# Performance work log

Hardware: AMD Instinct MI355X
Metric: run time of the kernel (lower is better)

The kernel has to match this reference:

```python
import jax, jax.numpy as jnp
import numpy as np

B, S, D = 4, 4096, 1024   # batch, seq_len, d_model
E, K, H = 8, 2, 2048      # num_experts, top_k, expert hidden dim


def setup_inputs() -> dict:
    key = jax.random.key(0)
    k0, k1, k2, k3, k4 = jax.random.split(key, 5)
    scale = 0.02
    return {
        "x": jax.random.normal(k0, (B, S, D), jnp.float32),
        "gate_w": jax.random.normal(k1, (D, E), jnp.float32) * scale,      # nn.Linear(d_model, E, bias=False)
        "w_gate": jax.random.normal(k2, (E, D, H), jnp.float32) * scale,   # expert SwiGLU gate proj
        "w_up":   jax.random.normal(k3, (E, D, H), jnp.float32) * scale,   # expert up proj
        "w_down": jax.random.normal(k4, (E, H, D), jnp.float32) * scale,   # expert down proj
    }


def reference(x, gate_w, w_gate, w_up, w_down):
    b, s, d = x.shape
    e = gate_w.shape[1]
    x_flat = x.reshape(-1, d)                          # [T, D], T = B*S

    gate_logits = x_flat @ gate_w                      # [T, E] (eval mode: no noise)
    top_logits, top_idx = jax.lax.top_k(gate_logits, K)  # [T, K]
    top_w = jax.nn.softmax(top_logits.astype(jnp.float32), axis=1).astype(x.dtype)  # [T, K]

    # load-balancing aux loss (Switch/Mixtral style)
    f_i = jax.nn.one_hot(top_idx, e, dtype=jnp.float32).sum(axis=1).mean(axis=0)  # [E]
    p_i = jax.nn.softmax(gate_logits, axis=1).mean(axis=0)                        # [E]
    aux_loss = (f_i * p_i).sum() * (e ** 2)

    flat_idx = top_idx.reshape(-1)                     # [T*K] expert ids
    # pre-scale token copies by routing weight (matches original)
    y = (x_flat[:, None, :] * top_w[:, :, None]).reshape(-1, d)  # [T*K, D]

    expert_out = jnp.zeros_like(y)
    for i in range(e):  # fixed small expert count: dense-fallback masked MLP
        h = jax.nn.silu(y @ w_gate[i]) * (y @ w_up[i])           # [T*K, H]
        o_i = h @ w_down[i]                                      # [T*K, D]
        expert_out = jnp.where((flat_idx == i)[:, None], o_i, expert_out)

    # faithful to original: scatter_add indexed by EXPERT id (as written in source)
    final = jnp.zeros_like(x_flat).at[flat_idx].add(expert_out)  # [T, D]
    return final.reshape(b, s, d), aux_loss
```

## Files before the change

### kernel.cpp

```cpp
#include <hip/hip_runtime.h>
#include <hip/hip_bf16.h>
#include <stdint.h>

#define T_TOK  16384
#define DMODEL 1024
#define NEXP   8
#define HDIM   2048
#define CAPSL  16512

#define BM 128
#define BN 128
#define NWORK_MAX 264
#define YROWS_MAX (NWORK_MAX*BM)
#define GRID_GEMM (NWORK_MAX * 16)

#define OFF_COUNTS 0
#define OFF_NWORK  64
#define OFF_FSUM   128
#define OFF_PSUM   192
#define OFF_WORK   256
#define OFF_HSUM   8192
#define OFF_ZERO_END 73728
#define OFF_TOK    131072
#define OFF_WGT    786432
#define OFF_WT     2097152
#define WT_ELEMS   (NEXP*HDIM*DMODEL)
#define OFF_Y      (OFF_WT + (size_t)2*WT_ELEMS*2)
#define NEED_FAST  (OFF_Y + (size_t)YROWS_MAX*DMODEL*2)

typedef __attribute__((ext_vector_type(4))) float f32x4;
typedef __attribute__((ext_vector_type(8))) short bf16x8;

__device__ __forceinline__ unsigned short f2bf(float f) {
    unsigned int u = __builtin_bit_cast(unsigned int, f);
    unsigned int r = (u + 0x7fffu + ((u >> 16) & 1u)) >> 16;
    return (unsigned short)r;
}

__global__ __launch_bounds__(256) void wt_fragment(const float* __restrict__ wg,
                                                   const float* __restrict__ wu,
                                                   unsigned short* __restrict__ wt_out) {
    int mat = blockIdx.z;
    const float* src = mat ? wu : wg;
    unsigned short* dst = wt_out + (size_t)mat * WT_ELEMS;
    int e  = blockIdx.y;
    int kt = blockIdx.x & 15;
    int ht = blockIdx.x >> 4;
    __shared__ unsigned short tile[64][68];
    const float* s = src + ((size_t)e * DMODEL + kt * 64) * HDIM + ht * 64;
    for (int u = threadIdx.x; u < 1024; u += 256) {
        int r = u >> 4, c = (u & 15) * 4;
        float4 v = *(const float4*)(s + (size_t)r * HDIM + c);
        tile[r][c + 0] = f2bf(v.x); tile[r][c + 1] = f2bf(v.y);
        tile[r][c + 2] = f2bf(v.z); tile[r][c + 3] = f2bf(v.w);
    }
    __syncthreads();
    for (int cc = threadIdx.x; cc < 512; cc += 256) {
        int r   = cc & 15;
        int q   = (cc >> 4) & 3;
        int sl  = (cc >> 6) & 1;
        int ntl = cc >> 7;
        int hh  = ntl * 16 + r;
        int ddb = sl * 32 + q * 8;
        bf16x8 o;
        #pragma unroll
        for (int j = 0; j < 8; ++j) o[j] = (short)tile[ddb + j][hh];
        size_t idx = ((((size_t)e * 128 + ht * 4 + ntl) * 32 + kt * 2 + sl) * 4 + q) * 128
                     + r * 8;
        *(bf16x8*)(dst + idx) = o;
    }
}

__global__ __launch_bounds__(256) void gating(const float* __restrict__ x,
                                              const float* __restrict__ gw,
                                              int* counts, float* fsum, float* psum,
                                              int* tok_list, float* wgt_list) {
    __shared__ float gws_t[NEXP * DMODEL];
    __shared__ int   ch_e[64][2];
    __shared__ float ch_w[64][2];
    __shared__ float pacc[NEXP];
    __shared__ int   hist[NEXP], gbase[NEXP], cursor[NEXP];
    if (threadIdx.x < NEXP) { pacc[threadIdx.x] = 0.f; hist[threadIdx.x] = 0; cursor[threadIdx.x] = 0; }
    for (int u = threadIdx.x; u < NEXP * DMODEL; u += 256) {
        gws_t[(u & 7) * DMODEL + (u >> 3)] = gw[u];
    }
    __syncthreads();
    int wave = threadIdx.x >> 6, lane = threadIdx.x & 63;
    int tbase = blockIdx.x * 64;
    for (int it = 0; it < 16; ++it) {
        int slot = wave * 16 + it;
        int t = tbase + slot;
        float p[8] = {0, 0, 0, 0, 0, 0, 0, 0};
        #pragma unroll
        for (int j = 0; j < 16; ++j) {
            float xv = x[(size_t)t * DMODEL + j * 64 + lane];
            #pragma unroll
            for (int e2 = 0; e2 < 8; ++e2) p[e2] += xv * gws_t[e2 * DMODEL + j * 64 + lane];
        }
        #pragma unroll
        for (int off = 32; off >= 1; off >>= 1) {
            #pragma unroll
            for (int e2 = 0; e2 < 8; ++e2) p[e2] += __shfl_xor(p[e2], off);
        }
        if (lane == 0) {
            int i0 = 0; float l0 = p[0];
            #pragma unroll
            for (int e2 = 1; e2 < 8; ++e2) if (p[e2] > l0) { l0 = p[e2]; i0 = e2; }
            int i1 = -1; float l1 = -1e30f;
            #pragma unroll
            for (int e2 = 0; e2 < 8; ++e2) if (e2 != i0 && p[e2] > l1) { l1 = p[e2]; i1 = e2; }
            float a = __expf(l1 - l0);
            float w0 = 1.f / (1.f + a);
            ch_e[slot][0] = i0; ch_e[slot][1] = i1;
            ch_w[slot][0] = w0; ch_w[slot][1] = a * w0;
            atomicAdd(&hist[i0], 1); atomicAdd(&hist[i1], 1);
            float s = 0.f, ex[8];
            #pragma unroll
            for (int e2 = 0; e2 < 8; ++e2) { ex[e2] = __expf(p[e2] - l0); s += ex[e2]; }
            float inv = 1.f / s;
            #pragma unroll
            for (int e2 = 0; e2 < 8; ++e2) atomicAdd(&pacc[e2], ex[e2] * inv);
        }
    }
    __syncthreads();
    if (threadIdx.x < NEXP) {
        int h = hist[threadIdx.x];
        gbase[threadIdx.x] = atomicAdd(&counts[threadIdx.x], h);
        atomicAdd(&fsum[threadIdx.x], (float)h);
        atomicAdd(&psum[threadIdx.x], pacc[threadIdx.x]);
    }
    __syncthreads();
    if (threadIdx.x < 64) {
        int slot = threadIdx.x, t = tbase + slot;
        #pragma unroll
        for (int k2 = 0; k2 < 2; ++k2) {
            int e2 = ch_e[slot][k2];
            int pos = gbase[e2] + atomicAdd(&cursor[e2], 1);
            tok_list[e2 * CAPSL + pos] = t;
            wgt_list[e2 * CAPSL + pos] = ch_w[slot][k2];
        }
    }
}

__global__ void build_work(const int* counts, int4* work, int* n_work,
                           const float* fsum, const float* psum, float* out_aux) {
    int lane = threadIdx.x;
    if (lane < NEXP) {
        int base_t = 0;
        for (int j = 0; j < lane; ++j) base_t += (counts[j] + BM - 1) / BM;
        int nt = (counts[lane] + BM - 1) / BM;
        for (int r = 0; r < nt; ++r)
            work[base_t + r] = make_int4(lane, r * BM, (base_t + r) * BM, 0);
        if (lane == NEXP - 1) *n_work = base_t + nt;
    }
    if (lane == 0) {
        float aux = 0.f;
        for (int e = 0; e < NEXP; ++e)
            aux += (fsum[e] / (float)T_TOK) * (psum[e] / (float)T_TOK);
        *out_aux = aux * (float)(NEXP * NEXP);
    }
}

__global__ __launch_bounds__(256) void materialize(const float* __restrict__ x,
                                                   const int* __restrict__ tok_list,
                                                   const float* __restrict__ wgt_list,
                                                   const int* __restrict__ counts,
                                                   const int4* __restrict__ work,
                                                   const int* __restrict__ n_work,
                                                   unsigned short* __restrict__ yfrag) {
    int w = blockIdx.x; if (w >= *n_work) return;
    int4 wi = work[w];
    int e = wi.x, row0 = wi.y, yb = wi.z;
    int cnt = counts[e];
    int rtb  = (yb >> 4) + blockIdx.y * 4;
    int rloc = blockIdx.y * 64;
    for (int v = threadIdx.x; v < 8192; v += 256) {
        int r   = v & 15;
        int q   = (v >> 4) & 3;
        int s   = (v >> 6) & 31;
        int rtl = v >> 11;
        int slot = row0 + rloc + rtl * 16 + r;
        bf16x8 o;
        if (slot < cnt) {
            int t = tok_list[e * CAPSL + slot];
            float wgt = wgt_list[e * CAPSL + slot];
            const float* xp = x + (size_t)t * DMODEL + s * 32 + q * 8;
            float4 v0 = *(const float4*)xp;
            float4 v1 = *(const float4*)(xp + 4);
            o[0] = f2bf(v0.x * wgt); o[1] = f2bf(v0.y * wgt);
            o[2] = f2bf(v0.z * wgt); o[3] = f2bf(v0.w * wgt);
            o[4] = f2bf(v1.x * wgt); o[5] = f2bf(v1.y * wgt);
            o[6] = f2bf(v1.z * wgt); o[7] = f2bf(v1.w * wgt);
        } else {
            #pragma unroll
            for (int j = 0; j < 8; ++j) o[j] = 0;
        }
        *(bf16x8*)(yfrag + (size_t)(rtb + rtl) * 16384 + (s * 4 + q) * 128 + r * 8) = o;
    }
}

#define MM_CLUSTER(AF, GF, UF) do {                                                    \
    __builtin_amdgcn_s_setprio(1);                                                     \
    _Pragma("unroll")                                                                  \
    for (int mi = 0; mi < 4; ++mi) {                                                   \
        _Pragma("unroll")                                                              \
        for (int ni = 0; ni < 4; ++ni) {                                               \
            accg[mi][ni] = __builtin_amdgcn_mfma_f32_16x16x32_bf16(AF[mi], GF[ni], accg[mi][ni], 0, 0, 0); \
            accu[mi][ni] = __builtin_amdgcn_mfma_f32_16x16x32_bf16(AF[mi], UF[ni], accu[mi][ni], 0, 0, 0); \
        }                                                                              \
    }                                                                                  \
    __builtin_amdgcn_s_setprio(0);                                                     \
} while (0)

__global__ __launch_bounds__(256, 2) void moe_gemm_fast(
        const unsigned short* __restrict__ yfrag,
        const unsigned short* __restrict__ wfrag,
        const int4* __restrict__ work, const int* __restrict__ n_work,
        float* __restrict__ hsum) {
    __shared__ float red[4][64];
    int bid = blockIdx.x;
    int xcd = bid & 7, idx = bid >> 3;
    int nbc = idx / 132;
    int rem = idx - nbc * 132;
    int w   = xcd * 33 + (rem >> 2);
    int nb  = nbc * 4 + (rem & 3);
    if (w >= *n_work) return;
    int4 wi = work[w];
    int e = wi.x, yb = wi.z;
    int tid = threadIdx.x, wave = tid >> 6, lane = tid & 63;
    int wm = wave >> 1, wn = wave & 1;

    const bf16x8* pA[4]; const bf16x8* pG[4]; const bf16x8* pU[4];
    #pragma unroll
    for (int mi = 0; mi < 4; ++mi)
        pA[mi] = (const bf16x8*)(yfrag + (size_t)((yb >> 4) + wm * 4 + mi) * 16384 + lane * 8);
    #pragma unroll
    for (int ni = 0; ni < 4; ++ni) {
        size_t nt = (size_t)e * 128 + nb * 8 + wn * 4 + ni;
        pG[ni] = (const bf16x8*)(wfrag + nt * 16384 + lane * 8);
        pU[ni] = (const bf16x8*)(wfrag + (size_t)WT_ELEMS + nt * 16384 + lane * 8);
    }

    f32x4 accg[4][4], accu[4][4];
    #pragma unroll
    for (int mi = 0; mi < 4; ++mi)
        #pragma unroll
        for (int ni = 0; ni < 4; ++ni) {
            accg[mi][ni] = (f32x4){0.f, 0.f, 0.f, 0.f};
            accu[mi][ni] = (f32x4){0.f, 0.f, 0.f, 0.f};
        }

    bf16x8 aA[4], gA[4], uA[4], aB[4], gB[4], uB[4];
    #pragma unroll
    for (int mi = 0; mi < 4; ++mi) aA[mi] = pA[mi][0];
    #pragma unroll
    for (int ni = 0; ni < 4; ++ni) { gA[ni] = pG[ni][0]; uA[ni] = pU[ni][0]; }

    #pragma unroll 1
    for (int s = 0; s < 32; s += 2) {
        {
            int o = (s + 1) * 64;
            #pragma unroll
            for (int mi = 0; mi < 4; ++mi) aB[mi] = pA[mi][o];
            #pragma unroll
            for (int ni = 0; ni < 4; ++ni) { gB[ni] = pG[ni][o]; uB[ni] = pU[ni][o]; }
        }
        MM_CLUSTER(aA, gA, uA);
        if (s + 2 < 32) {
            int o = (s + 2) * 64;
            #pragma unroll
            for (int mi = 0; mi < 4; ++mi) aA[mi] = pA[mi][o];
            #pragma unroll
            for (int ni = 0; ni < 4; ++ni) { gA[ni] = pG[ni][o]; uA[ni] = pU[ni][o]; }
        }
        MM_CLUSTER(aB, gB, uB);
    }

    #pragma unroll
    for (int ni = 0; ni < 4; ++ni) {
        float s = 0.f;
        #pragma unroll
        for (int mi = 0; mi < 4; ++mi)
            #pragma unroll
            for (int i = 0; i < 4; ++i) {
                float gv = accg[mi][ni][i], uv = accu[mi][ni][i];
                s += (gv / (1.f + __expf(-gv))) * uv;
            }
        s += __shfl_xor(s, 16);
        s += __shfl_xor(s, 32);
        if (lane < 16) red[wave][ni * 16 + lane] = s;
    }
    __syncthreads();
    if (tid < BN) {
        int wnc = tid >> 6, ix = tid & 63;
        float v = red[wnc][ix] + red[2 + wnc][ix];
        atomicAdd(&hsum[(size_t)e * HDIM + nb * 128 + tid], v);
    }
}

__global__ __launch_bounds__(256) void moe_slow(const float* __restrict__ x,
                                                const int* __restrict__ tok_list,
                                                const float* __restrict__ wgt_list,
                                                const int* __restrict__ counts,
                                                const float* __restrict__ wgate,
                                                const float* __restrict__ wup,
                                                float* __restrict__ hsum) {
    int e = blockIdx.x;
    int h = blockIdx.y * 256 + threadIdx.x;
    int cnt = counts[e];
    __shared__ float xs[DMODEL];
    float acc = 0.f;
    for (int i = 0; i < cnt; ++i) {
        int t = tok_list[e * CAPSL + i];
        float wv = wgt_list[e * CAPSL + i];
        for (int u = threadIdx.x; u < DMODEL; u += 256)
            xs[u] = x[(size_t)t * DMODEL + u] * wv;
        __syncthreads();
        float g = 0.f, uvv = 0.f;
        for (int k = 0; k < DMODEL; ++k) {
            float xv = xs[k];
            g   += xv * wgate[((size_t)e * DMODEL + k) * HDIM + h];
            uvv += xv * wup[((size_t)e * DMODEL + k) * HDIM + h];
        }
        acc += (g / (1.f + __expf(-g))) * uvv;
        __syncthreads();
    }
    atomicAdd(&hsum[(size_t)e * HDIM + h], acc);
}

__global__ __launch_bounds__(256) void down_proj(const float* __restrict__ hsum,
                                                 const float* __restrict__ wd,
                                                 float* __restrict__ out) {
    int e    = blockIdx.x;
    int dblk = blockIdx.y;
    int hblk = blockIdx.z;
    __shared__ float sh[256];
    int h0 = hblk * 256;
    sh[threadIdx.x] = hsum[(size_t)e * HDIM + h0 + threadIdx.x];
    __syncthreads();
    int d = dblk * 256 + threadIdx.x;
    const float* wp = wd + ((size_t)e * HDIM + h0) * DMODEL + d;
    float acc = 0.f;
    #pragma unroll 4
    for (int h = 0; h < 256; h += 4) {
        float4 s4 = *(const float4*)&sh[h];
        acc += s4.x * wp[(size_t)(h + 0) * DMODEL];
        acc += s4.y * wp[(size_t)(h + 1) * DMODEL];
        acc += s4.z * wp[(size_t)(h + 2) * DMODEL];
        acc += s4.w * wp[(size_t)(h + 3) * DMODEL];
    }
    atomicAdd(&out[(size_t)e * DMODEL + d], acc);
}

extern "C" void kernel_launch(void* const* d_in, const int* in_sizes, int n_in,
                              void* d_out, int out_size, void* d_ws, size_t ws_size,
                              hipStream_t stream) {
    const float* x     = (const float*)d_in[0];
    const float* gw    = (const float*)d_in[1];
    const float* wgate = (const float*)d_in[2];
    const float* wup   = (const float*)d_in[3];
    const float* wdown = (const float*)d_in[4];
    float* out = (float*)d_out;
    char*  ws  = (char*)d_ws;

    int*   counts = (int*)(ws + OFF_COUNTS);
    int*   nwork  = (int*)(ws + OFF_NWORK);
    float* fsum   = (float*)(ws + OFF_FSUM);
    float* psum   = (float*)(ws + OFF_PSUM);
    int4*  workv  = (int4*)(ws + OFF_WORK);
    float* hsum   = (float*)(ws + OFF_HSUM);
    int*   tok    = (int*)(ws + OFF_TOK);
    float* wgt    = (float*)(ws + OFF_WGT);
    unsigned short* wt   = (unsigned short*)(ws + OFF_WT);
    unsigned short* ybuf = (unsigned short*)(ws + OFF_Y);

    hipMemsetAsync(d_out, 0, (size_t)out_size * sizeof(float), stream);
    hipMemsetAsync(d_ws, 0, OFF_ZERO_END, stream);

    gating<<<256, 256, 0, stream>>>(x, gw, counts, fsum, psum, tok, wgt);
    build_work<<<1, 64, 0, stream>>>(counts, workv, nwork, fsum, psum,
                                     out + (size_t)T_TOK * DMODEL);

    bool fast = ws_size >= NEED_FAST;
    if (fast) {
        wt_fragment<<<dim3(512, 8, 2), 256, 0, stream>>>(wgate, wup, wt);
        materialize<<<dim3(NWORK_MAX, 2), 256, 0, stream>>>(x, tok, wgt, counts, workv, nwork, ybuf);
        moe_gemm_fast<<<dim3(GRID_GEMM), 256, 0, stream>>>(ybuf, wt, workv, nwork, hsum);
    } else {
        moe_slow<<<dim3(NEXP, HDIM / 256), 256, 0, stream>>>(x, tok, wgt, counts,
                                                             wgate, wup, hsum);
    }

    down_proj<<<dim3(NEXP, 4, 8), 256, 0, stream>>>(hsum, wdown, out);
}
```

Measured before the change: 415.6 us.

## Switch expert GEMM to 32x32x16 MFMA with matching fragment layouts

Replaces the 16x16x32 bf16 MFMA tiles in the fused gate/up GEMM with 32x32x16 MFMA instructions. The weight-fragment and activation-fragment pre-layout kernels are rewritten to produce 32-row/column tiles with 16-wide K slices. The epilogue reduction changes to match the new accumulator layout. The aim is fewer MFMA instructions and operand fetches per FLOP, at the cost of more accumulator registers per instruction and the risk of layout indexing errors.

```diff
diff --git a/kernel.cpp b/kernel.cpp
--- a/kernel.cpp
+++ b/kernel.cpp
@@ -28,8 +28,9 @@
 #define OFF_Y      (OFF_WT + (size_t)2*WT_ELEMS*2)
 #define NEED_FAST  (OFF_Y + (size_t)YROWS_MAX*DMODEL*2)
 
-typedef __attribute__((ext_vector_type(4))) float f32x4;
-typedef __attribute__((ext_vector_type(8))) short bf16x8;
+typedef __attribute__((ext_vector_type(4)))  float f32x4;
+typedef __attribute__((ext_vector_type(16))) float f32x16;
+typedef __attribute__((ext_vector_type(8)))  short bf16x8;
 
 __device__ __forceinline__ unsigned short f2bf(float f) {
     unsigned int u = __builtin_bit_cast(unsigned int, f);
@@ -56,17 +57,17 @@
     }
     __syncthreads();
     for (int cc = threadIdx.x; cc < 512; cc += 256) {
-        int r   = cc & 15;
-        int q   = (cc >> 4) & 3;
-        int sl  = (cc >> 6) & 1;
-        int ntl = cc >> 7;
-        int hh  = ntl * 16 + r;
-        int ddb = sl * 32 + q * 8;
+        int col  = cc & 31;
+        int kgrp = (cc >> 5) & 1;
+        int s16l = (cc >> 6) & 3;
+        int ntl  = cc >> 8;
+        int hh   = ntl * 32 + col;
+        int ddb  = s16l * 16 + kgrp * 8;
         bf16x8 o;
         #pragma unroll
         for (int j = 0; j < 8; ++j) o[j] = (short)tile[ddb + j][hh];
-        size_t idx = ((((size_t)e * 128 + ht * 4 + ntl) * 32 + kt * 2 + sl) * 4 + q) * 128
-                     + r * 8;
+        size_t idx = (((size_t)(e * 64 + ht * 2 + ntl)) * 64 + (kt * 4 + s16l)) * 512
+                     + (kgrp * 32 + col) * 8;
         *(bf16x8*)(dst + idx) = o;
     }
 }
@@ -172,19 +173,19 @@
     int4 wi = work[w];
     int e = wi.x, row0 = wi.y, yb = wi.z;
     int cnt = counts[e];
-    int rtb  = (yb >> 4) + blockIdx.y * 4;
+    int rtb  = (yb >> 5) + blockIdx.y * 2;
     int rloc = blockIdx.y * 64;
     for (int v = threadIdx.x; v < 8192; v += 256) {
-        int r   = v & 15;
-        int q   = (v >> 4) & 3;
-        int s   = (v >> 6) & 31;
-        int rtl = v >> 11;
-        int slot = row0 + rloc + rtl * 16 + r;
+        int row  = v & 31;
+        int kgrp = (v >> 5) & 1;
+        int s16  = (v >> 6) & 63;
+        int rtl  = v >> 12;
+        int slot = row0 + rloc + rtl * 32 + row;
         bf16x8 o;
         if (slot < cnt) {
             int t = tok_list[e * CAPSL + slot];
             float wgt = wgt_list[e * CAPSL + slot];
-            const float* xp = x + (size_t)t * DMODEL + s * 32 + q * 8;
+            const float* xp = x + (size_t)t * DMODEL + s16 * 16 + kgrp * 8;
             float4 v0 = *(const float4*)xp;
             float4 v1 = *(const float4*)(xp + 4);
             o[0] = f2bf(v0.x * wgt); o[1] = f2bf(v0.y * wgt);
@@ -195,18 +196,23 @@
             #pragma unroll
             for (int j = 0; j < 8; ++j) o[j] = 0;
         }
-        *(bf16x8*)(yfrag + (size_t)(rtb + rtl) * 16384 + (s * 4 + q) * 128 + r * 8) = o;
-    }
-}
+        *(bf16x8*)(yfrag + (size_t)(rtb + rtl) * 32768 + (size_t)s16 * 512
+                   + (kgrp * 32 + row) * 8) = o;
+    }
+}
+
+#define MFMA32(a, b, c) __builtin_amdgcn_mfma_f32_32x32x16_bf16(a, b, c, 0, 0, 0)
 
 #define MM_CLUSTER(AF, GF, UF) do {                                                    \
     __builtin_amdgcn_s_setprio(1);                                                     \
     _Pragma("unroll")                                                                  \
-    for (int mi = 0; mi < 4; ++mi) {                                                   \
+    for (int mi = 0; mi < 2; ++mi) {                                                   \
         _Pragma("unroll")                                                              \
-        for (int ni = 0; ni < 4; ++ni) {                                               \
-            accg[mi][ni] = __builtin_amdgcn_mfma_f32_16x16x32_bf16(AF[mi], GF[ni], accg[mi][ni], 0, 0, 0); \
-            accu[mi][ni] = __builtin_amdgcn_mfma_f32_16x16x32_bf16(AF[mi], UF[ni], accu[mi][ni], 0, 0, 0); \
+        for (int ni = 0; ni < 2; ++ni) {                                               \
+            accg[mi][ni] = MFMA32(AF[mi * 2 + 0], GF[ni * 2 + 0], accg[mi][ni]);       \
+            accu[mi][ni] = MFMA32(AF[mi * 2 + 0], UF[ni * 2 + 0], accu[mi][ni]);       \
+            accg[mi][ni] = MFMA32(AF[mi * 2 + 1], GF[ni * 2 + 1], accg[mi][ni]);       \
+            accu[mi][ni] = MFMA32(AF[mi * 2 + 1], UF[ni * 2 + 1], accu[mi][ni]);       \
         }                                                                              \
     }                                                                                  \
     __builtin_amdgcn_s_setprio(0);                                                     \
@@ -230,65 +236,84 @@
     int tid = threadIdx.x, wave = tid >> 6, lane = tid & 63;
     int wm = wave >> 1, wn = wave & 1;
 
-    const bf16x8* pA[4]; const bf16x8* pG[4]; const bf16x8* pU[4];
-    #pragma unroll
-    for (int mi = 0; mi < 4; ++mi)
-        pA[mi] = (const bf16x8*)(yfrag + (size_t)((yb >> 4) + wm * 4 + mi) * 16384 + lane * 8);
-    #pragma unroll
-    for (int ni = 0; ni < 4; ++ni) {
-        size_t nt = (size_t)e * 128 + nb * 8 + wn * 4 + ni;
-        pG[ni] = (const bf16x8*)(wfrag + nt * 16384 + lane * 8);
-        pU[ni] = (const bf16x8*)(wfrag + (size_t)WT_ELEMS + nt * 16384 + lane * 8);
-    }
-
-    f32x4 accg[4][4], accu[4][4];
-    #pragma unroll
-    for (int mi = 0; mi < 4; ++mi)
-        #pragma unroll
-        for (int ni = 0; ni < 4; ++ni) {
-            accg[mi][ni] = (f32x4){0.f, 0.f, 0.f, 0.f};
-            accu[mi][ni] = (f32x4){0.f, 0.f, 0.f, 0.f};
+    const bf16x8* pA[2]; const bf16x8* pG[2]; const bf16x8* pU[2];
+    #pragma unroll
+    for (int mi = 0; mi < 2; ++mi)
+        pA[mi] = (const bf16x8*)(yfrag + (size_t)((yb >> 5) + wm * 2 + mi) * 32768 + lane * 8);
+    #pragma unroll
+    for (int ni = 0; ni < 2; ++ni) {
+        size_t nt = (size_t)e * 64 + nb * 4 + wn * 2 + ni;
+        pG[ni] = (const bf16x8*)(wfrag + nt * 32768 + lane * 8);
+        pU[ni] = (const bf16x8*)(wfrag + (size_t)WT_ELEMS + nt * 32768 + lane * 8);
+    }
+
+    f32x16 accg[2][2], accu[2][2];
+    #pragma unroll
+    for (int mi = 0; mi < 2; ++mi)
+        #pragma unroll
+        for (int ni = 0; ni < 2; ++ni) {
+            #pragma unroll
+            for (int i = 0; i < 16; ++i) { accg[mi][ni][i] = 0.f; accu[mi][ni][i] = 0.f; }
         }
 
     bf16x8 aA[4], gA[4], uA[4], aB[4], gB[4], uB[4];
     #pragma unroll
-    for (int mi = 0; mi < 4; ++mi) aA[mi] = pA[mi][0];
-    #pragma unroll
-    for (int ni = 0; ni < 4; ++ni) { gA[ni] = pG[ni][0]; uA[ni] = pU[ni][0]; }
+    for (int mi = 0; mi < 2; ++mi)
+        #pragma unroll
+        for (int kh = 0; kh < 2; ++kh) aA[mi * 2 + kh] = pA[mi][kh * 64];
+    #pragma unroll
+    for (int ni = 0; ni < 2; ++ni)
+        #pragma unroll
+        for (int kh = 0; kh < 2; ++kh) {
+            gA[ni * 2 + kh] = pG[ni][kh * 64];
+            uA[ni * 2 + kh] = pU[ni][kh * 64];
+        }
 
     #pragma unroll 1
     for (int s = 0; s < 32; s += 2) {
+        int o1 = (s + 1) * 128, o2 = (s + 2) * 128;
         {
-            int o = (s + 1) * 64;
-            #pragma unroll
-            for (int mi = 0; mi < 4; ++mi) aB[mi] = pA[mi][o];
-            #pragma unroll
-            for (int ni = 0; ni < 4; ++ni) { gB[ni] = pG[ni][o]; uB[ni] = pU[ni][o]; }
+            #pragma unroll
+            for (int mi = 0; mi < 2; ++mi)
+                #pragma unroll
+                for (int kh = 0; kh < 2; ++kh) aB[mi * 2 + kh] = pA[mi][o1 + kh * 64];
+            #pragma unroll
+            for (int ni = 0; ni < 2; ++ni)
+                #pragma unroll
+                for (int kh = 0; kh < 2; ++kh) {
+                    gB[ni * 2 + kh] = pG[ni][o1 + kh * 64];
+                    uB[ni * 2 + kh] = pU[ni][o1 + kh * 64];
+                }
         }
         MM_CLUSTER(aA, gA, uA);
         if (s + 2 < 32) {
-            int o = (s + 2) * 64;
-            #pragma unroll
-            for (int mi = 0; mi < 4; ++mi) aA[mi] = pA[mi][o];
-            #pragma unroll
-            for (int ni = 0; ni < 4; ++ni) { gA[ni] = pG[ni][o]; uA[ni] = pU[ni][o]; }
+            #pragma unroll
+            for (int mi = 0; mi < 2; ++mi)
+                #pragma unroll
+                for (int kh = 0; kh < 2; ++kh) aA[mi * 2 + kh] = pA[mi][o2 + kh * 64];
+            #pragma unroll
+            for (int ni = 0; ni < 2; ++ni)
+                #pragma unroll
+                for (int kh = 0; kh < 2; ++kh) {
+                    gA[ni * 2 + kh] = pG[ni][o2 + kh * 64];
+                    uA[ni * 2 + kh] = pU[ni][o2 + kh * 64];
+                }
         }
         MM_CLUSTER(aB, gB, uB);
     }
 
     #pragma unroll
-    for (int ni = 0; ni < 4; ++ni) {
-        float s = 0.f;
-        #pragma unroll
-        for (int mi = 0; mi < 4; ++mi)
-            #pragma unroll
-            for (int i = 0; i < 4; ++i) {
+    for (int ni = 0; ni < 2; ++ni) {
+        float ssum = 0.f;
+        #pragma unroll
+        for (int mi = 0; mi < 2; ++mi)
+            #pragma unroll
+            for (int i = 0; i < 16; ++i) {
                 float gv = accg[mi][ni][i], uv = accu[mi][ni][i];
-                s += (gv / (1.f + __expf(-gv))) * uv;
+                ssum += (gv / (1.f + __expf(-gv))) * uv;
             }
-        s += __shfl_xor(s, 16);
-        s += __shfl_xor(s, 32);
-        if (lane < 16) red[wave][ni * 16 + lane] = s;
+        ssum += __shfl_xor(ssum, 32);
+        if (lane < 32) red[wave][ni * 32 + lane] = ssum;
     }
     __syncthreads();
     if (tid < BN) {
```

Result: slower. 462.2 us (+11.2%).
